# Kernel tuning notes

Hardware: AMD Instinct MI355X
Metric: run time of the kernel (lower is better)

## Reference

```python
import jax, jax.numpy as jnp
import numpy as np

ACT_DIM, H, ZD, NZ, B, T, NS = 20, 64, 64, 5, 1024, 128, 1000


def setup_inputs() -> dict:
    key = jax.random.key(0)
    ks = jax.random.split(key, 24)
    w = lambda k, s: jax.random.normal(k, s, jnp.float32) * 0.1
    return {
        'acts': jax.random.randint(ks[0], (B, T), 0, ACT_DIM, dtype=jnp.int32),
        'durs': jax.random.uniform(ks[1], (B, T), jnp.float32),
        'W_act': w(ks[2], (ACT_DIM, H)), 'b_act': jnp.zeros(H, jnp.float32),
        'W_dur': w(ks[3], (1, H)), 'b_dur': jnp.zeros(H, jnp.float32),
        'W_x': w(ks[4], (2 * H, H)), 'b_x': jnp.zeros(H, jnp.float32),
        'W_z': w(ks[5], (ZD, H)), 'b_z': jnp.zeros(H, jnp.float32),
        'Wp1': w(ks[6], (NZ, 2 * H, H)), 'bp1': jnp.zeros((NZ, H), jnp.float32),
        'Wp2': w(ks[7], (NZ, H, ZD)), 'bp2': jnp.zeros((NZ, ZD), jnp.float32),
        'Wq1': w(ks[8], (NZ, H, ZD)), 'bq1': jnp.zeros((NZ, ZD), jnp.float32),
        'Wq2': w(ks[9], (NZ, ZD, ZD)), 'bq2': jnp.zeros((NZ, ZD), jnp.float32),
        'W_dec': w(ks[10], (2 * H, H)), 'b_dec': jnp.zeros(H, jnp.float32),
        'W_a': w(ks[11], (H, ACT_DIM)), 'b_a': jnp.zeros(ACT_DIM, jnp.float32),
        'W_durd': w(ks[12], (2 * H, 1)), 'b_durd': jnp.zeros(1, jnp.float32),
        'W_ih': w(ks[13], (2 * H, 3 * H)), 'W_hh': w(ks[14], (H, 3 * H)),
        'b_ih': jnp.zeros(3 * H, jnp.float32), 'b_hh': jnp.zeros(3 * H, jnp.float32),
        'gamma_post': jnp.ones((1, NZ), jnp.float32),
        'gamma_prior': jnp.ones((1, NZ), jnp.float32),
    }


def reference(acts, durs, W_act, b_act, W_dur, b_dur, W_x, b_x, W_z, b_z,
              Wp1, bp1, Wp2, bp2, Wq1, bq1, Wq2, bq2, W_dec, b_dec,
              W_a, b_a, W_durd, b_durd, W_ih, W_hh, b_ih, b_hh,
              gamma_post, gamma_prior):
    relu, sp = jax.nn.relu, jax.nn.softplus
    Bn, Tn = acts.shape
    hd = W_hh.shape[0]
    rngkey = jax.random.key(42)

    # Precompute per-timestep input embeddings, vectorized over T.
    one_hot = jax.nn.one_hot(acts, W_act.shape[0], dtype=jnp.float32)   # (B,T,A)
    phi_act = relu(one_hot @ W_act + b_act)                              # (B,T,H)
    phi_dur = relu(durs[..., None] * W_dur[0] + b_dur)                   # (B,T,H)
    phi_x_all = relu(jnp.concatenate([phi_act, phi_dur], -1) @ W_x + b_x)
    phi_x_all = jnp.swapaxes(phi_x_all, 0, 1)                            # (T,B,H)

    # NOTE: the torch code computes mu and sigma from the SAME network output
    # (identical pre-activation), so we compute it once. gamma matmul: (1,nz)@(B,nz,z)->(B,1,z)
    def mix_post(inp):
        h1 = relu(jnp.einsum('bi,nio->bno', inp, Wp1) + bp1)
        pre = jnp.einsum('bno,noz->bnz', h1, Wp2) + bp2
        m = jnp.einsum('on,bnz->boz', gamma_post, pre)
        return relu(m), sp(m)

    def mix_prior(h):
        h1 = relu(jnp.einsum('bi,nio->bno', h, Wq1) + bq1)
        pre = jnp.einsum('bno,noz->bnz', h1, Wq2) + bq2
        m = jnp.einsum('on,bnz->boz', gamma_prior, pre)
        return relu(m), sp(m)

    def gru(x, h):
        gi = x @ W_ih + b_ih
        gh = h @ W_hh + b_hh
        ir, iz, inn = jnp.split(gi, 3, -1)
        hr, hz, hn = jnp.split(gh, 3, -1)
        r = jax.nn.sigmoid(ir + hr)
        zz = jax.nn.sigmoid(iz + hz)
        n = jnp.tanh(inn + r * hn)
        return (1.0 - zz) * n + zz * h

    def sample_mean(k, mu, sigma):
        eps = jnp.mean(jax.random.normal(k, (NS,) + mu.shape, mu.dtype), 0)
        return (mu + sigma * eps)[:, 0, :]

    def kl(m1, s1, m2, s2):  # diag-normal KL, summed over z (Independent, 1)
        return jnp.sum(jnp.log(s2 / s1) + (s1 ** 2 + (m1 - m2) ** 2) / (2.0 * s2 ** 2) - 0.5, -1)

    def step(carry, xs):
        h, kld = carry
        phi_x, t = xs
        pm, ps = mix_post(jnp.concatenate([phi_x, h], -1))
        qm, qs = mix_prior(h)
        kld = kld + kl(pm, ps, qm, qs)
        z = sample_mean(jax.random.fold_in(rngkey, t), pm, ps)
        phi_z = relu(z @ W_z + b_z)
        h = gru(jnp.concatenate([phi_x, phi_z], -1), h)
        return (h, kld), None

    h0 = jnp.zeros((Bn, hd), jnp.float32)
    (h, kld), _ = jax.lax.scan(step, (h0, jnp.zeros((Bn, 1), jnp.float32)),
                               (phi_x_all, jnp.arange(Tn)))

    qm, qs = mix_prior(h)
    z = sample_mean(jax.random.fold_in(rngkey, Tn), qm, qs)
    phi_z = relu(z @ W_z + b_z)
    dec = relu(jnp.concatenate([phi_z, h], -1) @ W_dec + b_dec)
    logits = dec @ W_a + b_a
    phi_logits = relu(logits @ W_act + b_act)
    dur_dec = jnp.concatenate([phi_logits, dec], -1) @ W_durd + b_durd
    return logits, (dur_dec, sp(dur_dec)), jnp.mean(kld)
```

## Files before the change

kernel.cpp:

```cpp
#include <hip/hip_runtime.h>
#include <hip/hip_bf16.h>
#include <math.h>


#define TT   128
#define NZN  5
#define ADIM 20
#define ROWS 16
#define FRW  36
#define PS   68
#define PHIX_OFF (8 * FRW * 64 * 8)

typedef __attribute__((ext_vector_type(8))) short short8;
typedef __attribute__((ext_vector_type(4))) float f32x4;

__device__ __forceinline__ float reluf(float x) { return fmaxf(x, 0.f); }
__device__ __forceinline__ float frcp(float x)  { return __builtin_amdgcn_rcpf(x); }
__device__ __forceinline__ float fexp(float x)  { return __expf(x); }
__device__ __forceinline__ float flog(float x)  { return __logf(x); }
__device__ __forceinline__ float fsigm(float x) { return frcp(1.f + fexp(-x)); }
__device__ __forceinline__ float ftanh(float x) {
    float cx = fminf(fmaxf(x, -15.f), 15.f);
    float e2 = fexp(2.f * cx);
    return 1.f - 2.f * frcp(e2 + 1.f);
}
__device__ __forceinline__ float fsoftplus(float x) {
    return fmaxf(x, 0.f) + flog(1.f + fexp(-fabsf(x)));
}
__device__ __forceinline__ unsigned int pk2bf(float lo, float hi) {
    unsigned int r;
    asm volatile("v_cvt_pk_bf16_f32 %0, %1, %2" : "=v"(r) : "v"(lo), "v"(hi));
    return r;
}
__device__ __forceinline__ void stage2(short* buf, int shift, int rw0, int col,
                                       float v0, float v1) {
    unsigned int u = pk2bf(v0, v1);
    buf[(rw0 << shift) + (col ^ ((rw0 & 7) << 3))]             = (short)(u & 0xffff);
    buf[((rw0 + 1) << shift) + (col ^ (((rw0 + 1) & 7) << 3))] = (short)(u >> 16);
}
__device__ __forceinline__ short8 lda64(const short* b, int c, int col0) {
    return *(const short8*)(b + c * 64 + (col0 ^ ((c & 7) << 3)));
}
__device__ __forceinline__ short8 lda128(const short* b, int c, int col0) {
    return *(const short8*)(b + c * 128 + (col0 ^ ((c & 7) << 3)));
}
__device__ __forceinline__ unsigned short f2bf(float x) {
    union { float f; unsigned int u; } v; v.f = x;
    unsigned int r = v.u + 0x7fffu + ((v.u >> 16) & 1u);
    return (unsigned short)(r >> 16);
}
__device__ __forceinline__ float wave_sum64(float v) {
#pragma unroll
    for (int off = 32; off > 0; off >>= 1) v += __shfl_xor(v, off, 64);
    return v;
}
#define MFMA(a, b, acc) __builtin_amdgcn_mfma_f32_16x16x32_bf16((a), (b), (acc), 0, 0, 0)

__global__ void vrnn_zero(float* out) { out[22528] = 0.f; }

__global__ __launch_bounds__(256) void vrnn_pack(
    const float* __restrict__ Wp1, const float* __restrict__ Wq1,
    const float* __restrict__ Wp2, const float* __restrict__ Wq2,
    const float* __restrict__ W_z, const float* __restrict__ W_ih,
    const float* __restrict__ W_hh, short* __restrict__ ws)
{
    const int tid = blockIdx.x * blockDim.x + threadIdx.x;
    if (tid >= 8 * FRW * 64) return;
    const int l = tid & 63, f = (tid >> 6) % FRW, w = (tid >> 6) / FRW;
    const int cc = l & 15, gg = l >> 4;
    const float* src = nullptr; int ld = 64, ncol = 0, k0 = 0;
    if (w < 4) {
        const int fcp = 16 * w + cc; ncol = fcp;
        if (f < 16)      { int n = f >> 2, q = f & 3;
                           src = Wp1 + n * 8192; k0 = 32 * q; }
        else if (f < 26) { int r = f - 16; int n = r >> 1, q = r & 1;
                           src = Wp2 + n * 4096; k0 = 32 * q; }
        else if (f < 28) { src = W_z;  k0 = 32 * (f - 26); }
        else if (f < 34) { int r = f - 28; int gt = r >> 1, q = r & 1;
                           src = W_ih; ld = 192; ncol = gt * 64 + fcp; k0 = 64 + 32 * q; }
    } else {
        const int fcp = 16 * (w - 4) + cc; ncol = fcp;
        if (f < 10)      { int n = f >> 1, q = f & 1;
                           src = Wq1 + n * 4096; k0 = 32 * q; }
        else if (f < 16) { int r = f - 10; int gt = r >> 1, q = r & 1;
                           src = W_hh; ld = 192; ncol = gt * 64 + fcp; k0 = 32 * q; }
        else if (f < 20) { src = Wp1 + 4 * 8192; k0 = 32 * (f - 16); }
        else if (f < 30) { int r = f - 20; int n = r >> 1, q = r & 1;
                           src = Wq2 + n * 4096; k0 = 32 * q; }
        else             { int r = f - 30; int gt = r >> 1, q = r & 1;
                           src = W_ih; ld = 192; ncol = gt * 64 + fcp; k0 = 32 * q; }
    }
    short8 frag = {0, 0, 0, 0, 0, 0, 0, 0};
    if (src) {
#pragma unroll
        for (int j = 0; j < 8; ++j)
            frag[j] = (short)f2bf(src[(k0 + 8 * gg + j) * ld + ncol]);
    }
    *(short8*)(ws + ((w * FRW + f) * 64 + l) * 8) = frag;
}

__global__ __launch_bounds__(256) void phix_prep(
    const int* __restrict__ acts, const float* __restrict__ durs,
    const float* __restrict__ W_act, const float* __restrict__ b_act,
    const float* __restrict__ W_dur, const float* __restrict__ b_dur,
    const float* __restrict__ W_x,  const float* __restrict__ b_x,
    short* __restrict__ phix)
{
    const int blk = blockIdx.x >> 3, tch = blockIdx.x & 7;
    const int tid = threadIdx.x, v = tid >> 6, l = tid & 63;
    __shared__ float sWx[8192];
    __shared__ float scat[4][128];
    for (int e = tid; e < 8192; e += 256) sWx[e] = W_x[e];
    const float bact = b_act[l], wdur = W_dur[l], bdur = b_dur[l], bx = b_x[l];
    __syncthreads();
    for (int u = 0; u < 64; ++u) {
        const int pp = v * 64 + u;
        const int t = tch * 16 + (pp >> 4);
        const int r = pp & 15;
        const int b = blk * 16 + r;
        const int   a   = acts[b * TT + t];
        const float dur = durs[b * TT + t];
        scat[v][l]      = reluf(W_act[a * 64 + l] + bact);
        scat[v][64 + l] = reluf(fmaf(dur, wdur, bdur));
        __syncthreads();
        float phi = bx;
#pragma unroll 8
        for (int i = 0; i < 128; ++i)
            phi = fmaf(scat[v][i], sWx[i * 64 + l], phi);
        phix[((t * 64 + blk) * 16 + r) * 64 + (l ^ ((r & 7) << 3))] =
            (short)f2bf(reluf(phi));
        __syncthreads();
    }
}

__global__ __launch_bounds__(512, 1) void vrnn_main(
    const float* __restrict__ W_act, const float* __restrict__ b_act,
    const float* __restrict__ b_z,
    const float* __restrict__ bp1, const float* __restrict__ bq1,
    const float* __restrict__ bp2, const float* __restrict__ bq2,
    const float* __restrict__ b_ih, const float* __restrict__ b_hh,
    const float* __restrict__ g_post, const float* __restrict__ g_prior,
    const float* __restrict__ Wq1, const float* __restrict__ Wq2,
    const float* __restrict__ W_z, const float* __restrict__ W_dec,
    const float* __restrict__ b_dec, const float* __restrict__ W_a,
    const float* __restrict__ b_a, const float* __restrict__ W_durd,
    const float* __restrict__ b_durd,
    const short* __restrict__ ws, float* __restrict__ d_out)
{
    const int w = threadIdx.x >> 6, l = threadIdx.x & 63;
    const bool isH = (w >= 4);
    const int ns = isH ? (w - 4) : w;
    const int g = l >> 4, c = l & 15;
    const int fc = 16 * ns + c;
    const int row0 = blockIdx.x * ROWS;
    const short* __restrict__ phix = ws + PHIX_OFF;

    __shared__ __align__(16) short s_xz[ROWS * 128];
    __shared__ __align__(16) short s_h[ROWS * 64];
    __shared__ __align__(16) short s_h1p[NZN][ROWS * 64];
    __shared__ __align__(16) short s_h1q[NZN][ROWS * 64];
    __shared__ __align__(16) short s_z[ROWS * 64];
    __shared__ float s_gh[3][ROWS * PS];
    __shared__ float s_gix[3][ROWS * PS];
    __shared__ float s_qm[ROWS * PS], s_qs[ROWS * PS], s_lqs[ROWS * PS];
    __shared__ float s_hf[ROWS * 64];
    __shared__ float s_fin[8][320];
    __shared__ float s_klsum[ROWS];

    const short8* Bw = ((const short8*)ws) + (w * FRW) * 64 + l;
#define BF(f) Bw[(f) * 64]
    const f32x4 Z4 = {0.f, 0.f, 0.f, 0.f};

    float b1r[NZN], gam[NZN];
    float c2 = 0.f, bA = 0.f, bzr = 0.f;
    if (!isH) {
#pragma unroll
        for (int n = 0; n < NZN; ++n) {
            gam[n] = g_post[n];
            b1r[n] = bp1[n * 64 + fc];
            c2 = fmaf(gam[n], bp2[n * 64 + fc], c2);
        }
        bzr = b_z[fc];
    } else {
#pragma unroll
        for (int n = 0; n < NZN; ++n) {
            gam[n] = g_prior[n];
            b1r[n] = bq1[n * 64 + fc];
            c2 = fmaf(gam[n], bq2[n * 64 + fc], c2);
        }
        bA = bp1[4 * 64 + fc];
    }
    const float bih0 = b_ih[fc], bih1 = b_ih[64 + fc], bih2 = b_ih[128 + fc];
    const float bhh0 = b_hh[fc], bhh1 = b_hh[64 + fc], bhh2 = b_hh[128 + fc];

    float hr[4] = {0.f, 0.f, 0.f, 0.f};
    float kl[4] = {0.f, 0.f, 0.f, 0.f};
    float pmv[4];

    for (int i = threadIdx.x; i < ROWS * 64; i += 512) s_h[i] = 0;
    if (threadIdx.x < ROWS) s_klsum[threadIdx.x] = 0.f;

    short8 ax0, ax1, ah0, ah1;

    for (int t = 0; t < TT; ++t) {
        __syncthreads();
        if (!isH) {
            const int idx = w * 64 + l;
            const int r  = idx >> 4;
            const int c0 = (idx & 15) * 4;
            const uint2* src = (const uint2*)(phix + (size_t)(t * 64 + blockIdx.x) * 1024);
            uint2 val = src[idx];
            *(uint2*)(s_xz + r * 128 + c0) = val;
        } else {
            ah0 = lda64(s_h, c, 8 * g);
            ah1 = lda64(s_h, c, 32 + 8 * g);
#pragma unroll
            for (int n = 0; n < NZN; ++n) {
                f32x4 q = MFMA(ah0, BF(2 * n), Z4);
                q = MFMA(ah1, BF(2 * n + 1), q);
                stage2(s_h1q[n], 6, 4 * g,     fc, reluf(q[0] + b1r[n]), reluf(q[1] + b1r[n]));
                stage2(s_h1q[n], 6, 4 * g + 2, fc, reluf(q[2] + b1r[n]), reluf(q[3] + b1r[n]));
            }
#pragma unroll
            for (int gt = 0; gt < 3; ++gt) {
                f32x4 gh = MFMA(ah0, BF(10 + 2 * gt), Z4);
                gh = MFMA(ah1, BF(11 + 2 * gt), gh);
#pragma unroll
                for (int r = 0; r < 4; ++r)
                    s_gh[gt][(4 * g + r) * PS + fc] = gh[r];
            }
        }
        __syncthreads();
        if (!isH) {
            ax0 = lda128(s_xz, c, 8 * g);
            ax1 = lda128(s_xz, c, 32 + 8 * g);
            ah0 = lda64(s_h, c, 8 * g);
            ah1 = lda64(s_h, c, 32 + 8 * g);
#pragma unroll
            for (int n = 0; n < 4; ++n) {
                f32x4 p = MFMA(ax0, BF(4 * n + 0), Z4);
                p = MFMA(ax1, BF(4 * n + 1), p);
                p = MFMA(ah0, BF(4 * n + 2), p);
                p = MFMA(ah1, BF(4 * n + 3), p);
                stage2(s_h1p[n], 6, 4 * g,     fc, reluf(p[0] + b1r[n]), reluf(p[1] + b1r[n]));
                stage2(s_h1p[n], 6, 4 * g + 2, fc, reluf(p[2] + b1r[n]), reluf(p[3] + b1r[n]));
            }
        } else {
            ax0 = lda128(s_xz, c, 8 * g);
            ax1 = lda128(s_xz, c, 32 + 8 * g);
            {
                f32x4 p = MFMA(ax0, BF(16), Z4);
                p = MFMA(ax1, BF(17), p);
                p = MFMA(ah0, BF(18), p);
                p = MFMA(ah1, BF(19), p);
                stage2(s_h1p[4], 6, 4 * g,     fc, reluf(p[0] + bA), reluf(p[1] + bA));
                stage2(s_h1p[4], 6, 4 * g + 2, fc, reluf(p[2] + bA), reluf(p[3] + bA));
            }
            f32x4 mq = Z4;
#pragma unroll
            for (int n = 0; n < NZN; ++n) {
                short8 hq0 = lda64(s_h1q[n], c, 8 * g);
                short8 hq1 = lda64(s_h1q[n], c, 32 + 8 * g);
                f32x4 q = MFMA(hq0, BF(20 + 2 * n), Z4);
                q = MFMA(hq1, BF(21 + 2 * n), q);
#pragma unroll
                for (int r = 0; r < 4; ++r) mq[r] = fmaf(gam[n], q[r], mq[r]);
            }
#pragma unroll
            for (int r = 0; r < 4; ++r) {
                const int rw = 4 * g + r;
                float mpri = mq[r] + c2;
                float qm = reluf(mpri), qs = fsoftplus(mpri);
                s_qm[rw * PS + fc] = qm;
                s_qs[rw * PS + fc] = qs;
                s_lqs[rw * PS + fc] = flog(qs);
            }
        }
        __syncthreads();
        if (!isH) {
            f32x4 mp = Z4;
#pragma unroll
            for (int n = 0; n < NZN; ++n) {
                short8 hp0 = lda64(s_h1p[n], c, 8 * g);
                short8 hp1 = lda64(s_h1p[n], c, 32 + 8 * g);
                f32x4 p = MFMA(hp0, BF(16 + 2 * n), Z4);
                p = MFMA(hp1, BF(17 + 2 * n), p);
#pragma unroll
                for (int r = 0; r < 4; ++r) mp[r] = fmaf(gam[n], p[r], mp[r]);
            }
#pragma unroll
            for (int r = 0; r < 4; ++r) {
                const int rw = 4 * g + r;
                float mpost = mp[r] + c2;
                float pm = reluf(mpost), ps = fsoftplus(mpost);
                float qm = s_qm[rw * PS + fc];
                float qs = s_qs[rw * PS + fc];
                float lqs = s_lqs[rw * PS + fc];
                float dd = pm - qm;
                kl[r] += lqs - flog(ps) + (ps * ps + dd * dd) * 0.5f * frcp(qs * qs) - 0.5f;
                pmv[r] = pm;
            }
            stage2(s_z, 6, 4 * g,     fc, pmv[0], pmv[1]);
            stage2(s_z, 6, 4 * g + 2, fc, pmv[2], pmv[3]);
        } else {
#pragma unroll
            for (int gt = 0; gt < 3; ++gt) {
                f32x4 gx = MFMA(ax0, BF(30 + 2 * gt), Z4);
                gx = MFMA(ax1, BF(31 + 2 * gt), gx);
#pragma unroll
                for (int r = 0; r < 4; ++r)
                    s_gix[gt][(4 * g + r) * PS + fc] = gx[r];
            }
        }
        __syncthreads();
        if (!isH) {
            short8 az0 = lda64(s_z, c, 8 * g);
            short8 az1 = lda64(s_z, c, 32 + 8 * g);
            f32x4 zz = MFMA(az0, BF(26), Z4);
            zz = MFMA(az1, BF(27), zz);
            stage2(s_xz, 7, 4 * g,     64 + fc, reluf(zz[0] + bzr), reluf(zz[1] + bzr));
            stage2(s_xz, 7, 4 * g + 2, 64 + fc, reluf(zz[2] + bzr), reluf(zz[3] + bzr));
        }
        __syncthreads();
        if (!isH) {
            short8 gz0 = lda128(s_xz, c, 64 + 8 * g);
            short8 gz1 = lda128(s_xz, c, 96 + 8 * g);
            f32x4 gi0 = MFMA(gz0, BF(28), Z4); gi0 = MFMA(gz1, BF(29), gi0);
            f32x4 gi1 = MFMA(gz0, BF(30), Z4); gi1 = MFMA(gz1, BF(31), gi1);
            f32x4 gi2 = MFMA(gz0, BF(32), Z4); gi2 = MFMA(gz1, BF(33), gi2);
#pragma unroll
            for (int r = 0; r < 4; ++r) {
                const int rw = 4 * g + r;
                float i0 = gi0[r] + s_gix[0][rw * PS + fc] + bih0;
                float i1 = gi1[r] + s_gix[1][rw * PS + fc] + bih1;
                float i2 = gi2[r] + s_gix[2][rw * PS + fc] + bih2;
                float h0 = s_gh[0][rw * PS + fc] + bhh0;
                float h1 = s_gh[1][rw * PS + fc] + bhh1;
                float h2 = s_gh[2][rw * PS + fc] + bhh2;
                float rr = fsigm(i0 + h0);
                float zg = fsigm(i1 + h1);
                float nn = ftanh(i2 + rr * h2);
                hr[r] = (1.f - zg) * nn + zg * hr[r];
            }
            stage2(s_h, 6, 4 * g,     fc, hr[0], hr[1]);
            stage2(s_h, 6, 4 * g + 2, fc, hr[2], hr[3]);
        }
    }

    if (!isH) {
#pragma unroll
        for (int r = 0; r < 4; ++r) s_hf[(4 * g + r) * 64 + fc] = hr[r];
#pragma unroll
        for (int off = 1; off < 16; off <<= 1) {
#pragma unroll
            for (int r = 0; r < 4; ++r) kl[r] += __shfl_xor(kl[r], off, 64);
        }
        if (c == 0) {
#pragma unroll
            for (int r = 0; r < 4; ++r) atomicAdd(&s_klsum[4 * g + r], kl[r]);
        }
    }
    __syncthreads();

    {
        float gqe[NZN];
#pragma unroll
        for (int n = 0; n < NZN; ++n) gqe[n] = g_prior[n];
        float* sf = s_fin[w];
        for (int rr = 0; rr < 2; ++rr) {
            const int lr = 2 * w + rr, grow = row0 + lr;
            float accn[NZN];
#pragma unroll
            for (int n = 0; n < NZN; ++n) accn[n] = bq1[n * 64 + l];
            for (int i = 0; i < 64; ++i) {
                const float hv = s_hf[lr * 64 + i];
#pragma unroll
                for (int n = 0; n < NZN; ++n) accn[n] += hv * Wq1[(n * 64 + i) * 64 + l];
            }
#pragma unroll
            for (int n = 0; n < NZN; ++n) sf[n * 64 + l] = reluf(accn[n]);
            float u[NZN];
#pragma unroll
            for (int n = 0; n < NZN; ++n) u[n] = bq2[n * 64 + l];
            for (int o = 0; o < 64; ++o) {
#pragma unroll
                for (int n = 0; n < NZN; ++n) u[n] += sf[n * 64 + o] * Wq2[(n * 64 + o) * 64 + l];
            }
            float mpri = 0.f;
#pragma unroll
            for (int n = 0; n < NZN; ++n) mpri = fmaf(gqe[n], u[n], mpri);
            sf[l] = reluf(mpri);
            float za = b_z[l];
            for (int i = 0; i < 64; ++i) za += sf[i] * W_z[i * 64 + l];
            sf[64 + l] = reluf(za);
            float dv = b_dec[l];
            for (int i = 0; i < 64; ++i) {
                dv += sf[64 + i] * W_dec[i * 64 + l];
                dv += s_hf[lr * 64 + i] * W_dec[(64 + i) * 64 + l];
            }
            const float dec = reluf(dv);
            sf[128 + l] = dec;
            float lg = 0.f;
            if (l < ADIM) {
                lg = b_a[l];
                for (int o = 0; o < 64; ++o) lg += sf[128 + o] * W_a[o * ADIM + l];
                d_out[grow * ADIM + l] = lg;
                sf[192 + l] = lg;
            }
            float pl = b_act[l];
#pragma unroll
            for (int j = 0; j < ADIM; ++j) pl += sf[192 + j] * W_act[j * 64 + l];
            pl = reluf(pl);
            float contrib = pl * W_durd[l] + dec * W_durd[64 + l];
            contrib = wave_sum64(contrib);
            if (l == 0) {
                const float dd = contrib + b_durd[0];
                d_out[20480 + grow] = dd;
                d_out[21504 + grow] = fsoftplus(dd);
            }
        }
    }
    if (threadIdx.x == 0) {
        float s = 0.f;
#pragma unroll
        for (int i = 0; i < ROWS; ++i) s += s_klsum[i];
        atomicAdd(d_out + 22528, s * (1.f / 1024.f));
    }
#undef BF
}

extern "C" void kernel_launch(void* const* d_in, const int* in_sizes, int n_in,
                              void* d_out, int out_size, void* d_ws, size_t ws_size,
                              hipStream_t stream)
{
    const int*   acts    = (const int*)  d_in[0];
    const float* durs    = (const float*)d_in[1];
    const float* W_act   = (const float*)d_in[2];
    const float* b_act   = (const float*)d_in[3];
    const float* W_dur   = (const float*)d_in[4];
    const float* b_dur   = (const float*)d_in[5];
    const float* W_x     = (const float*)d_in[6];
    const float* b_x     = (const float*)d_in[7];
    const float* W_z     = (const float*)d_in[8];
    const float* b_z     = (const float*)d_in[9];
    const float* Wp1     = (const float*)d_in[10];
    const float* bp1     = (const float*)d_in[11];
    const float* Wp2     = (const float*)d_in[12];
    const float* bp2     = (const float*)d_in[13];
    const float* Wq1     = (const float*)d_in[14];
    const float* bq1     = (const float*)d_in[15];
    const float* Wq2     = (const float*)d_in[16];
    const float* bq2     = (const float*)d_in[17];
    const float* W_dec   = (const float*)d_in[18];
    const float* b_dec   = (const float*)d_in[19];
    const float* W_a     = (const float*)d_in[20];
    const float* b_a     = (const float*)d_in[21];
    const float* W_durd  = (const float*)d_in[22];
    const float* b_durd  = (const float*)d_in[23];
    const float* W_ih    = (const float*)d_in[24];
    const float* W_hh    = (const float*)d_in[25];
    const float* b_ih    = (const float*)d_in[26];
    const float* b_hh    = (const float*)d_in[27];
    const float* g_post  = (const float*)d_in[28];
    const float* g_prior = (const float*)d_in[29];
    float* out = (float*)d_out;
    short* ws  = (short*)d_ws;

    vrnn_zero<<<1, 1, 0, stream>>>(out);
    vrnn_pack<<<72, 256, 0, stream>>>(Wp1, Wq1, Wp2, Wq2, W_z, W_ih, W_hh, ws);
    phix_prep<<<512, 256, 0, stream>>>(acts, durs, W_act, b_act, W_dur, b_dur,
                                       W_x, b_x, ws + PHIX_OFF);
    vrnn_main<<<64, 512, 0, stream>>>(
        W_act, b_act, b_z, bp1, bq1, bp2, bq2, b_ih, b_hh, g_post, g_prior,
        Wq1, Wq2, W_z, W_dec, b_dec, W_a, b_a, W_durd, b_durd,
        ws, out);
}
```

Baseline: 798.1 us.

## Merge prep kernels and drop a per-step barrier by splitting phi_z per wave

```diff
diff --git a/kernel.cpp b/kernel.cpp
--- a/kernel.cpp
+++ b/kernel.cpp
@@ -7,7 +7,7 @@
 #define NZN  5
 #define ADIM 20
 #define ROWS 16
-#define FRW  36
+#define FRW  40
 #define PS   68
 #define PHIX_OFF (8 * FRW * 64 * 8)
 
@@ -56,80 +56,90 @@
 }
 #define MFMA(a, b, acc) __builtin_amdgcn_mfma_f32_16x16x32_bf16((a), (b), (acc), 0, 0, 0)
 
-__global__ void vrnn_zero(float* out) { out[22528] = 0.f; }
-
-__global__ __launch_bounds__(256) void vrnn_pack(
-    const float* __restrict__ Wp1, const float* __restrict__ Wq1,
-    const float* __restrict__ Wp2, const float* __restrict__ Wq2,
-    const float* __restrict__ W_z, const float* __restrict__ W_ih,
-    const float* __restrict__ W_hh, short* __restrict__ ws)
-{
-    const int tid = blockIdx.x * blockDim.x + threadIdx.x;
-    if (tid >= 8 * FRW * 64) return;
-    const int l = tid & 63, f = (tid >> 6) % FRW, w = (tid >> 6) / FRW;
-    const int cc = l & 15, gg = l >> 4;
-    const float* src = nullptr; int ld = 64, ncol = 0, k0 = 0;
-    if (w < 4) {
-        const int fcp = 16 * w + cc; ncol = fcp;
-        if (f < 16)      { int n = f >> 2, q = f & 3;
-                           src = Wp1 + n * 8192; k0 = 32 * q; }
-        else if (f < 26) { int r = f - 16; int n = r >> 1, q = r & 1;
-                           src = Wp2 + n * 4096; k0 = 32 * q; }
-        else if (f < 28) { src = W_z;  k0 = 32 * (f - 26); }
-        else if (f < 34) { int r = f - 28; int gt = r >> 1, q = r & 1;
-                           src = W_ih; ld = 192; ncol = gt * 64 + fcp; k0 = 64 + 32 * q; }
-    } else {
-        const int fcp = 16 * (w - 4) + cc; ncol = fcp;
-        if (f < 10)      { int n = f >> 1, q = f & 1;
-                           src = Wq1 + n * 4096; k0 = 32 * q; }
-        else if (f < 16) { int r = f - 10; int gt = r >> 1, q = r & 1;
-                           src = W_hh; ld = 192; ncol = gt * 64 + fcp; k0 = 32 * q; }
-        else if (f < 20) { src = Wp1 + 4 * 8192; k0 = 32 * (f - 16); }
-        else if (f < 30) { int r = f - 20; int n = r >> 1, q = r & 1;
-                           src = Wq2 + n * 4096; k0 = 32 * q; }
-        else             { int r = f - 30; int gt = r >> 1, q = r & 1;
-                           src = W_ih; ld = 192; ncol = gt * 64 + fcp; k0 = 32 * q; }
-    }
-    short8 frag = {0, 0, 0, 0, 0, 0, 0, 0};
-    if (src) {
-#pragma unroll
-        for (int j = 0; j < 8; ++j)
-            frag[j] = (short)f2bf(src[(k0 + 8 * gg + j) * ld + ncol]);
-    }
-    *(short8*)(ws + ((w * FRW + f) * 64 + l) * 8) = frag;
-}
-
-__global__ __launch_bounds__(256) void phix_prep(
+__global__ __launch_bounds__(256) void prep_all(
     const int* __restrict__ acts, const float* __restrict__ durs,
     const float* __restrict__ W_act, const float* __restrict__ b_act,
     const float* __restrict__ W_dur, const float* __restrict__ b_dur,
     const float* __restrict__ W_x,  const float* __restrict__ b_x,
-    short* __restrict__ phix)
+    const float* __restrict__ Wp1, const float* __restrict__ Wq1,
+    const float* __restrict__ Wp2, const float* __restrict__ Wq2,
+    const float* __restrict__ W_z, const float* __restrict__ W_ih,
+    const float* __restrict__ W_hh,
+    short* __restrict__ ws, float* __restrict__ out)
 {
-    const int blk = blockIdx.x >> 3, tch = blockIdx.x & 7;
-    const int tid = threadIdx.x, v = tid >> 6, l = tid & 63;
     __shared__ float sWx[8192];
     __shared__ float scat[4][128];
-    for (int e = tid; e < 8192; e += 256) sWx[e] = W_x[e];
+
+    if (blockIdx.x == 0 && threadIdx.x == 0) out[22528] = 0.f;
+
+    if (blockIdx.x < 80) {
+        const int tid = blockIdx.x * 256 + threadIdx.x;
+        const int l = tid & 63, f = (tid >> 6) % FRW, w = (tid >> 6) / FRW;
+        const int cc = l & 15, gg = l >> 4;
+        const float* src = nullptr; int ld = 64, ncol = 0, k0 = 0;
+        if (w < 4) {
+            const int fcp = 16 * w + cc;
+            if (f < 16)      { int n = f >> 2, q = f & 3;
+                               src = Wp1 + n * 8192; k0 = 32 * q; ncol = fcp; }
+            else if (f < 26) { int r = f - 16; int n = r >> 1, q = r & 1;
+                               src = Wp2 + n * 4096; k0 = 32 * q; ncol = fcp; }
+            else if (f < 34) { int r = f - 26; int s = r >> 1, q = r & 1;
+                               src = W_z; k0 = 32 * q; ncol = 16 * s + cc; }
+            else             { int r = f - 34; int gt = r >> 1, q = r & 1;
+                               src = W_ih; ld = 192; ncol = gt * 64 + fcp; k0 = 64 + 32 * q; }
+        } else {
+            const int fcp = 16 * (w - 4) + cc; ncol = fcp;
+            if (f < 10)      { int n = f >> 1, q = f & 1;
+                               src = Wq1 + n * 4096; k0 = 32 * q; }
+            else if (f < 16) { int r = f - 10; int gt = r >> 1, q = r & 1;
+                               src = W_hh; ld = 192; ncol = gt * 64 + fcp; k0 = 32 * q; }
+            else if (f < 20) { src = Wp1 + 4 * 8192; k0 = 32 * (f - 16); }
+            else if (f < 30) { int r = f - 20; int n = r >> 1, q = r & 1;
+                               src = Wq2 + n * 4096; k0 = 32 * q; }
+            else if (f < 36) { int r = f - 30; int gt = r >> 1, q = r & 1;
+                               src = W_ih; ld = 192; ncol = gt * 64 + fcp; k0 = 32 * q; }
+        }
+        short8 frag = {0, 0, 0, 0, 0, 0, 0, 0};
+        if (src) {
+#pragma unroll
+            for (int j = 0; j < 8; ++j)
+                frag[j] = (short)f2bf(src[(k0 + 8 * gg + j) * ld + ncol]);
+        }
+        *(short8*)(ws + ((w * FRW + f) * 64 + l) * 8) = frag;
+        return;
+    }
+
+    const int pb = blockIdx.x - 80;
+    const int blk = pb >> 3, tch = pb & 7;
+    const int v = threadIdx.x >> 6, l = threadIdx.x & 63;
+    short* __restrict__ phix = ws + PHIX_OFF;
+    for (int e = threadIdx.x; e < 8192; e += 256) sWx[e] = W_x[e];
     const float bact = b_act[l], wdur = W_dur[l], bdur = b_dur[l], bx = b_x[l];
     __syncthreads();
+    int a_n; float d_n;
+    {
+        const int pp = v * 64;
+        const int t0 = tch * 16 + (pp >> 4), b0 = blk * 16 + (pp & 15);
+        a_n = acts[b0 * TT + t0]; d_n = durs[b0 * TT + t0];
+    }
     for (int u = 0; u < 64; ++u) {
         const int pp = v * 64 + u;
         const int t = tch * 16 + (pp >> 4);
         const int r = pp & 15;
-        const int b = blk * 16 + r;
-        const int   a   = acts[b * TT + t];
-        const float dur = durs[b * TT + t];
+        const int a = a_n; const float dur = d_n;
+        if (u < 63) {
+            const int pp2 = pp + 1;
+            const int t2 = tch * 16 + (pp2 >> 4), b2 = blk * 16 + (pp2 & 15);
+            a_n = acts[b2 * TT + t2]; d_n = durs[b2 * TT + t2];
+        }
         scat[v][l]      = reluf(W_act[a * 64 + l] + bact);
         scat[v][64 + l] = reluf(fmaf(dur, wdur, bdur));
-        __syncthreads();
         float phi = bx;
 #pragma unroll 8
         for (int i = 0; i < 128; ++i)
             phi = fmaf(scat[v][i], sWx[i * 64 + l], phi);
         phix[((t * 64 + blk) * 16 + r) * 64 + (l ^ ((r & 7) << 3))] =
             (short)f2bf(reluf(phi));
-        __syncthreads();
     }
 }
 
@@ -162,9 +172,8 @@
     __shared__ __align__(16) short s_z[ROWS * 64];
     __shared__ float s_gh[3][ROWS * PS];
     __shared__ float s_gix[3][ROWS * PS];
-    __shared__ float s_qm[ROWS * PS], s_qs[ROWS * PS], s_lqs[ROWS * PS];
+    __shared__ float s_mp[ROWS * PS];
     __shared__ float s_hf[ROWS * 64];
-    __shared__ float s_fin[8][320];
     __shared__ float s_klsum[ROWS];
 
     const short8* Bw = ((const short8*)ws) + (w * FRW) * 64 + l;
@@ -172,7 +181,8 @@
     const f32x4 Z4 = {0.f, 0.f, 0.f, 0.f};
 
     float b1r[NZN], gam[NZN];
-    float c2 = 0.f, bA = 0.f, bzr = 0.f;
+    float c2 = 0.f, bA = 0.f;
+    float bzv[4] = {0.f, 0.f, 0.f, 0.f};
     if (!isH) {
 #pragma unroll
         for (int n = 0; n < NZN; ++n) {
@@ -180,7 +190,8 @@
             b1r[n] = bp1[n * 64 + fc];
             c2 = fmaf(gam[n], bp2[n * 64 + fc], c2);
         }
-        bzr = b_z[fc];
+#pragma unroll
+        for (int s = 0; s < 4; ++s) bzv[s] = b_z[16 * s + c];
     } else {
 #pragma unroll
         for (int n = 0; n < NZN; ++n) {
@@ -193,9 +204,9 @@
     const float bih0 = b_ih[fc], bih1 = b_ih[64 + fc], bih2 = b_ih[128 + fc];
     const float bhh0 = b_hh[fc], bhh1 = b_hh[64 + fc], bhh2 = b_hh[128 + fc];
 
-    float hr[4] = {0.f, 0.f, 0.f, 0.f};
-    float kl[4] = {0.f, 0.f, 0.f, 0.f};
-    float pmv[4];
+    float hr[4]  = {0.f, 0.f, 0.f, 0.f};
+    float kl[4]  = {0.f, 0.f, 0.f, 0.f};
+    float qmr[4], qsr[4], lqr[4];
 
     for (int i = threadIdx.x; i < ROWS * 64; i += 512) s_h[i] = 0;
     if (threadIdx.x < ROWS) s_klsum[threadIdx.x] = 0.f;
@@ -268,12 +279,10 @@
             }
 #pragma unroll
             for (int r = 0; r < 4; ++r) {
-                const int rw = 4 * g + r;
                 float mpri = mq[r] + c2;
-                float qm = reluf(mpri), qs = fsoftplus(mpri);
-                s_qm[rw * PS + fc] = qm;
-                s_qs[rw * PS + fc] = qs;
-                s_lqs[rw * PS + fc] = flog(qs);
+                qmr[r] = reluf(mpri);
+                qsr[r] = fsoftplus(mpri);
+                lqr[r] = flog(qsr[r]);
             }
         }
         __syncthreads();
@@ -288,17 +297,13 @@
 #pragma unroll
                 for (int r = 0; r < 4; ++r) mp[r] = fmaf(gam[n], p[r], mp[r]);
             }
+            float pmv[4];
 #pragma unroll
             for (int r = 0; r < 4; ++r) {
                 const int rw = 4 * g + r;
                 float mpost = mp[r] + c2;
-                float pm = reluf(mpost), ps = fsoftplus(mpost);
-                float qm = s_qm[rw * PS + fc];
-                float qs = s_qs[rw * PS + fc];
-                float lqs = s_lqs[rw * PS + fc];
-                float dd = pm - qm;
-                kl[r] += lqs - flog(ps) + (ps * ps + dd * dd) * 0.5f * frcp(qs * qs) - 0.5f;
-                pmv[r] = pm;
+                s_mp[rw * PS + fc] = mpost;
+                pmv[r] = reluf(mpost);
             }
             stage2(s_z, 6, 4 * g,     fc, pmv[0], pmv[1]);
             stage2(s_z, 6, 4 * g + 2, fc, pmv[2], pmv[3]);
@@ -314,20 +319,21 @@
         }
         __syncthreads();
         if (!isH) {
+            short* priv = ((short*)s_h1q) + ns * 1024;
             short8 az0 = lda64(s_z, c, 8 * g);
             short8 az1 = lda64(s_z, c, 32 + 8 * g);
-            f32x4 zz = MFMA(az0, BF(26), Z4);
-            zz = MFMA(az1, BF(27), zz);
-            stage2(s_xz, 7, 4 * g,     64 + fc, reluf(zz[0] + bzr), reluf(zz[1] + bzr));
-            stage2(s_xz, 7, 4 * g + 2, 64 + fc, reluf(zz[2] + bzr), reluf(zz[3] + bzr));
-        }
-        __syncthreads();
-        if (!isH) {
-            short8 gz0 = lda128(s_xz, c, 64 + 8 * g);
-            short8 gz1 = lda128(s_xz, c, 96 + 8 * g);
-            f32x4 gi0 = MFMA(gz0, BF(28), Z4); gi0 = MFMA(gz1, BF(29), gi0);
-            f32x4 gi1 = MFMA(gz0, BF(30), Z4); gi1 = MFMA(gz1, BF(31), gi1);
-            f32x4 gi2 = MFMA(gz0, BF(32), Z4); gi2 = MFMA(gz1, BF(33), gi2);
+#pragma unroll
+            for (int s = 0; s < 4; ++s) {
+                f32x4 zz = MFMA(az0, BF(26 + 2 * s), Z4);
+                zz = MFMA(az1, BF(27 + 2 * s), zz);
+                stage2(priv, 6, 4 * g,     16 * s + c, reluf(zz[0] + bzv[s]), reluf(zz[1] + bzv[s]));
+                stage2(priv, 6, 4 * g + 2, 16 * s + c, reluf(zz[2] + bzv[s]), reluf(zz[3] + bzv[s]));
+            }
+            short8 gz0 = lda64(priv, c, 8 * g);
+            short8 gz1 = lda64(priv, c, 32 + 8 * g);
+            f32x4 gi0 = MFMA(gz0, BF(34), Z4); gi0 = MFMA(gz1, BF(35), gi0);
+            f32x4 gi1 = MFMA(gz0, BF(36), Z4); gi1 = MFMA(gz1, BF(37), gi1);
+            f32x4 gi2 = MFMA(gz0, BF(38), Z4); gi2 = MFMA(gz1, BF(39), gi2);
 #pragma unroll
             for (int r = 0; r < 4; ++r) {
                 const int rw = 4 * g + r;
@@ -344,12 +350,23 @@
             }
             stage2(s_h, 6, 4 * g,     fc, hr[0], hr[1]);
             stage2(s_h, 6, 4 * g + 2, fc, hr[2], hr[3]);
+        } else {
+#pragma unroll
+            for (int r = 0; r < 4; ++r) {
+                const int rw = 4 * g + r;
+                float mpost = s_mp[rw * PS + fc];
+                float pm = reluf(mpost), ps = fsoftplus(mpost);
+                float dd = pm - qmr[r];
+                kl[r] += lqr[r] - flog(ps)
+                       + (ps * ps + dd * dd) * 0.5f * frcp(qsr[r] * qsr[r]) - 0.5f;
+            }
         }
     }
 
     if (!isH) {
 #pragma unroll
         for (int r = 0; r < 4; ++r) s_hf[(4 * g + r) * 64 + fc] = hr[r];
+    } else {
 #pragma unroll
         for (int off = 1; off < 16; off <<= 1) {
 #pragma unroll
@@ -366,7 +383,7 @@
         float gqe[NZN];
 #pragma unroll
         for (int n = 0; n < NZN; ++n) gqe[n] = g_prior[n];
-        float* sf = s_fin[w];
+        float* sf = ((float*)s_h1p) + w * 320;
         for (int rr = 0; rr < 2; ++rr) {
             const int lr = 2 * w + rr, grow = row0 + lr;
             float accn[NZN];
@@ -466,10 +483,9 @@
     float* out = (float*)d_out;
     short* ws  = (short*)d_ws;
 
-    vrnn_zero<<<1, 1, 0, stream>>>(out);
-    vrnn_pack<<<72, 256, 0, stream>>>(Wp1, Wq1, Wp2, Wq2, W_z, W_ih, W_hh, ws);
-    phix_prep<<<512, 256, 0, stream>>>(acts, durs, W_act, b_act, W_dur, b_dur,
-                                       W_x, b_x, ws + PHIX_OFF);
+    prep_all<<<592, 256, 0, stream>>>(acts, durs, W_act, b_act, W_dur, b_dur,
+                                      W_x, b_x, Wp1, Wq1, Wp2, Wq2, W_z, W_ih,
+                                      W_hh, ws, out);
     vrnn_main<<<64, 512, 0, stream>>>(
         W_act, b_act, b_z, bp1, bq1, bp2, bq2, b_ih, b_hh, g_post, g_prior,
         Wq1, Wq2, W_z, W_dec, b_dec, W_a, b_a, W_durd, b_durd,
```

Result: no change. 799.4 us (+0.2%).
